# Performance work log

Hardware: AMD Instinct MI355X
Metric: run time of the kernel (lower is better)

## Reference

```python
import jax, jax.numpy as jnp
import numpy as np

N_NODES = 50000
N_EDGES = 800000
IN_DIM = 128
HID = 128
N_GRAPHS = 64


def setup_inputs() -> dict:
    key = jax.random.key(0)
    ks = jax.random.split(key, 12)
    edge_index = jax.random.randint(ks[0], (2, N_EDGES), 0, N_NODES, dtype=jnp.int64)
    edge_weight = jax.random.uniform(ks[1], (N_EDGES,), dtype=jnp.float32)
    input_feature = jax.random.normal(ks[2], (N_NODES, IN_DIM), dtype=jnp.float32)
    graph_indicator = jnp.sort(jax.random.randint(ks[3], (N_NODES,), 0, N_GRAPHS, dtype=jnp.int64))
    s = 0.05
    W1 = jax.random.normal(ks[4], (IN_DIM, HID), dtype=jnp.float32) * s
    b1 = jnp.zeros((HID,), jnp.float32)
    W2 = jax.random.normal(ks[5], (HID, HID), dtype=jnp.float32) * s
    b2 = jnp.zeros((HID,), jnp.float32)
    W3 = jax.random.normal(ks[6], (HID, HID), dtype=jnp.float32) * s
    b3 = jnp.zeros((HID,), jnp.float32)
    wa = jax.random.normal(ks[7], (3 * HID, 1), dtype=jnp.float32) * s
    ba = jnp.zeros((1,), jnp.float32)
    Wf = jax.random.normal(ks[8], (3 * HID * 2, IN_DIM), dtype=jnp.float32) * s
    bf = jnp.zeros((IN_DIM,), jnp.float32)
    return dict(edge_index=edge_index, edge_weight=edge_weight,
                input_feature=input_feature, graph_indicator=graph_indicator,
                W1=W1, b1=b1, W2=W2, b2=b2, W3=W3, b3=b3,
                wa=wa, ba=ba, Wf=Wf, bf=bf)


def reference(edge_index, edge_weight, input_feature, graph_indicator,
              W1, b1, W2, b2, W3, b3, wa, ba, Wf, bf):
    src, dst = edge_index[0], edge_index[1]

    def gcn(x, W, b):
        # GraphConvolution: adj @ (x @ W) + b, adj given as weighted edge list
        support = x @ W  # [N, d_out]
        msg = edge_weight[:, None] * support[src]  # [E, d_out] gather
        return jax.ops.segment_sum(msg, dst, num_segments=N_NODES) + b

    g1 = jax.nn.relu(gcn(input_feature, W1, b1))
    g2 = jax.nn.relu(gcn(g1, W2, b2))
    g3 = jax.nn.relu(gcn(g2, W3, b3))
    h = jnp.concatenate([g1, g2, g3], axis=1)  # [N, 3*HID]

    # SelfAttentionPooling: attention score via a 1-dim GraphConvolution, tanh gate
    score = jnp.tanh(gcn(h, wa, ba))  # [N, 1]
    pool = h * score

    # segment avg / max pooling per graph
    seg_sum = jax.ops.segment_sum(pool, graph_indicator, num_segments=N_GRAPHS)
    counts = jax.ops.segment_sum(jnp.ones((N_NODES, 1), pool.dtype), graph_indicator,
                                 num_segments=N_GRAPHS)
    avg = seg_sum / jnp.maximum(counts, 1.0)
    mx = jax.ops.segment_max(pool, graph_indicator, num_segments=N_GRAPHS)
    pooled = jnp.concatenate([avg, mx], axis=1)  # [G, 6*HID]

    return jax.nn.relu(pooled @ Wf + bf)  # [G, IN_DIM]
```

## Files before the change

kernel.cpp:

```cpp
#include <hip/hip_runtime.h>
#include <math.h>

#define HID 128
#define POOL_SEG 16
#define WT_STRIDE 136
#define ELL_D 48
#define SC_CHUNK 2048
#define FXS 16384.0f
#define FXI (1.0f/16384.0f)
#define FG_KC 12

typedef __attribute__((ext_vector_type(8))) short short8;
typedef __attribute__((ext_vector_type(4))) float float4v;

__device__ inline short f2bf(float f) {
  unsigned u = __builtin_bit_cast(unsigned, f);
  unsigned r = (u + 0x7fff + ((u >> 16) & 1)) >> 16;
  return (short)r;
}
__device__ inline unsigned pack2bf(float lo, float hi) {
  return (unsigned)(unsigned short)f2bf(lo) | ((unsigned)(unsigned short)f2bf(hi) << 16);
}
__device__ inline float bflo(unsigned u) { return __builtin_bit_cast(float, u << 16); }
__device__ inline float bfhi(unsigned u) { return __builtin_bit_cast(float, u & 0xffff0000u); }
__device__ inline float bf2f(unsigned short s) { return __builtin_bit_cast(float, (unsigned)s << 16); }

__global__ void detect_flags(const int* __restrict__ ei, const int* __restrict__ gi,
                             int* __restrict__ flags, int n_nodes) {
  if (blockIdx.x == 0 && threadIdx.x == 0) {
    int nz = 0;
    for (int i = 1; i < 64; i += 2) nz |= ei[i];
    flags[0] = (nz == 0) ? 1 : 0;
    flags[1] = (gi[n_nodes - 1] == 0) ? 1 : 0;
  }
}

__global__ void prep_edges(const void* __restrict__ ei_raw, const int* __restrict__ flags,
                           const float* __restrict__ ew, int* __restrict__ dst32,
                           int2* __restrict__ sw, int E) {
  int e = blockIdx.x * blockDim.x + threadIdx.x;
  if (e >= E) return;
  int s, d;
  if (flags[0]) {
    const long long* p = (const long long*)ei_raw;
    s = (int)p[e]; d = (int)p[E + e];
  } else {
    const int* p = (const int*)ei_raw;
    s = p[e]; d = p[E + e];
  }
  dst32[e] = d;
  sw[e] = make_int2(s, __builtin_bit_cast(int, ew[e]));
}

__global__ void scatter_ell(const int* __restrict__ dst32, const int2* __restrict__ sw,
                            int* __restrict__ cursor, int2* __restrict__ ell, int E, int N) {
  int group = blockIdx.x & 7;
  int chunk = blockIdx.x >> 3;
  int rng = (N + 7) / 8;
  int lo = group * rng;
  int hi = lo + rng; if (hi > N) hi = N;
  int base = chunk * SC_CHUNK;
  for (int i = 0; i < SC_CHUNK; i += 256) {
    int e = base + i + threadIdx.x;
    if (e < E) {
      int d = dst32[e];
      if (d >= lo && d < hi) {
        int2 r = sw[e];
        int pos = atomicAdd(&cursor[d], 1);
        if (pos < ELL_D)
          ell[(size_t)d * ELL_D + pos] = r;
      }
    }
  }
}

__global__ void convert_w(const float* __restrict__ W1, const float* __restrict__ W2,
                          const float* __restrict__ W3, short* __restrict__ T1,
                          short* __restrict__ T2, short* __restrict__ T3) {
  int i = blockIdx.x * blockDim.x + threadIdx.x;
  int which = i >> 14, idx = i & 16383;
  int k = idx >> 7, n = idx & 127;
  const float* W = (which == 0) ? W1 : ((which == 1) ? W2 : W3);
  short* T = (which == 0) ? T1 : ((which == 1) ? T2 : T3);
  T[n * WT_STRIDE + k] = f2bf(W[idx]);
}

__global__ __launch_bounds__(256) void gemm_mfma(const float* __restrict__ Af,
                                                 const unsigned short* __restrict__ Abf,
                                                 const short* __restrict__ Wt,
                                                 unsigned short* __restrict__ C,
                                                 int n, int a_is_bf16) {
  __shared__ short Wlds[128 * WT_STRIDE];
  int t = threadIdx.x;
  {
    const ulonglong2* gsrc = (const ulonglong2*)Wt;
    ulonglong2* ldst = (ulonglong2*)Wlds;
    for (int i = t; i < (128 * WT_STRIDE) / 8; i += 256) ldst[i] = gsrc[i];
  }
  __syncthreads();

  int wave = t >> 6, lane = t & 63;
  int quad = lane >> 4, l15 = lane & 15;
  int m0 = blockIdx.x * 64 + wave * 16;

  int m = m0 + l15; if (m >= n) m = n - 1;
  short8 afrag[4];
  if (a_is_bf16) {
    const unsigned short* Arow = Abf + (size_t)m * 128;
#pragma unroll
    for (int c = 0; c < 4; c++) afrag[c] = *(const short8*)(Arow + c * 32 + quad * 8);
  } else {
    const float* Arow = Af + (size_t)m * 128;
#pragma unroll
    for (int c = 0; c < 4; c++) {
      int k0 = c * 32 + quad * 8;
      float4 x = *(const float4*)(Arow + k0);
      float4 y = *(const float4*)(Arow + k0 + 4);
      short8 a;
      a[0] = f2bf(x.x); a[1] = f2bf(x.y); a[2] = f2bf(x.z); a[3] = f2bf(x.w);
      a[4] = f2bf(y.x); a[5] = f2bf(y.y); a[6] = f2bf(y.z); a[7] = f2bf(y.w);
      afrag[c] = a;
    }
  }

  float4v acc[8];
#pragma unroll
  for (int tt = 0; tt < 8; tt++) acc[tt] = (float4v){0.f, 0.f, 0.f, 0.f};

#pragma unroll
  for (int c = 0; c < 4; c++) {
    int kb = c * 32 + quad * 8;
#pragma unroll
    for (int tt = 0; tt < 8; tt++) {
      const short8* bp = (const short8*)&Wlds[(tt * 16 + l15) * WT_STRIDE + kb];
      acc[tt] = __builtin_amdgcn_mfma_f32_16x16x32_bf16(afrag[c], *bp, acc[tt], 0, 0, 0);
    }
  }

  int rbase = m0 + quad * 4;
#pragma unroll
  for (int tt = 0; tt < 8; tt++) {
    int col = tt * 16 + l15;
#pragma unroll
    for (int r = 0; r < 4; r++) {
      int row = rbase + r;
      if (row < n) C[(size_t)row * 128 + col] = (unsigned short)f2bf(acc[tt][r]);
    }
  }
}

__global__ void aggregate(const unsigned short* __restrict__ support,
                          const int* __restrict__ deg_arr,
                          const int2* __restrict__ ell,
                          const float* __restrict__ bias, unsigned short* __restrict__ out,
                          const unsigned short* __restrict__ g1p,
                          const unsigned short* __restrict__ g2p,
                          const float* __restrict__ wa,
                          float* __restrict__ s_pre,
                          int n, int do_score) {
  int gid = blockIdx.x * blockDim.x + threadIdx.x;
  int node = gid >> 4, q = gid & 15;
  if (node >= n) return;
  int deg = deg_arr[node]; if (deg > ELL_D) deg = ELL_D;
  const int2* row = ell + (size_t)node * ELL_D;
  int acc[8];
#pragma unroll
  for (int j = 0; j < 8; j++) acc[j] = 0;
  const uint4* s4 = (const uint4*)support;

  int i = 0;
  for (; i + 3 < deg; i += 4) {
    int2 r0 = row[i], r1 = row[i + 1], r2 = row[i + 2], r3 = row[i + 3];
    float w0 = __builtin_bit_cast(float, r0.y) * FXS;
    float w1 = __builtin_bit_cast(float, r1.y) * FXS;
    float w2 = __builtin_bit_cast(float, r2.y) * FXS;
    float w3 = __builtin_bit_cast(float, r3.y) * FXS;
    uint4 v0 = s4[(size_t)r0.x * 16 + q];
    uint4 v1 = s4[(size_t)r1.x * 16 + q];
    uint4 v2 = s4[(size_t)r2.x * 16 + q];
    uint4 v3 = s4[(size_t)r3.x * 16 + q];
    acc[0] += __float2int_rn(w0 * bflo(v0.x)); acc[1] += __float2int_rn(w0 * bfhi(v0.x));
    acc[2] += __float2int_rn(w0 * bflo(v0.y)); acc[3] += __float2int_rn(w0 * bfhi(v0.y));
    acc[4] += __float2int_rn(w0 * bflo(v0.z)); acc[5] += __float2int_rn(w0 * bfhi(v0.z));
    acc[6] += __float2int_rn(w0 * bflo(v0.w)); acc[7] += __float2int_rn(w0 * bfhi(v0.w));
    acc[0] += __float2int_rn(w1 * bflo(v1.x)); acc[1] += __float2int_rn(w1 * bfhi(v1.x));
    acc[2] += __float2int_rn(w1 * bflo(v1.y)); acc[3] += __float2int_rn(w1 * bfhi(v1.y));
    acc[4] += __float2int_rn(w1 * bflo(v1.z)); acc[5] += __float2int_rn(w1 * bfhi(v1.z));
    acc[6] += __float2int_rn(w1 * bflo(v1.w)); acc[7] += __float2int_rn(w1 * bfhi(v1.w));
    acc[0] += __float2int_rn(w2 * bflo(v2.x)); acc[1] += __float2int_rn(w2 * bfhi(v2.x));
    acc[2] += __float2int_rn(w2 * bflo(v2.y)); acc[3] += __float2int_rn(w2 * bfhi(v2.y));
    acc[4] += __float2int_rn(w2 * bflo(v2.z)); acc[5] += __float2int_rn(w2 * bfhi(v2.z));
    acc[6] += __float2int_rn(w2 * bflo(v2.w)); acc[7] += __float2int_rn(w2 * bfhi(v2.w));
    acc[0] += __float2int_rn(w3 * bflo(v3.x)); acc[1] += __float2int_rn(w3 * bfhi(v3.x));
    acc[2] += __float2int_rn(w3 * bflo(v3.y)); acc[3] += __float2int_rn(w3 * bfhi(v3.y));
    acc[4] += __float2int_rn(w3 * bflo(v3.z)); acc[5] += __float2int_rn(w3 * bfhi(v3.z));
    acc[6] += __float2int_rn(w3 * bflo(v3.w)); acc[7] += __float2int_rn(w3 * bfhi(v3.w));
  }
  for (; i < deg; i++) {
    int2 r0 = row[i];
    float w0 = __builtin_bit_cast(float, r0.y) * FXS;
    uint4 v0 = s4[(size_t)r0.x * 16 + q];
    acc[0] += __float2int_rn(w0 * bflo(v0.x)); acc[1] += __float2int_rn(w0 * bfhi(v0.x));
    acc[2] += __float2int_rn(w0 * bflo(v0.y)); acc[3] += __float2int_rn(w0 * bfhi(v0.y));
    acc[4] += __float2int_rn(w0 * bflo(v0.z)); acc[5] += __float2int_rn(w0 * bfhi(v0.z));
    acc[6] += __float2int_rn(w0 * bflo(v0.w)); acc[7] += __float2int_rn(w0 * bfhi(v0.w));
  }

  float f[8];
#pragma unroll
  for (int j = 0; j < 8; j++) f[j] = (float)acc[j] * FXI;

  float4 b0 = ((const float4*)bias)[q * 2];
  float4 b1 = ((const float4*)bias)[q * 2 + 1];
  f[0] = fmaxf(f[0] + b0.x, 0.f); f[1] = fmaxf(f[1] + b0.y, 0.f);
  f[2] = fmaxf(f[2] + b0.z, 0.f); f[3] = fmaxf(f[3] + b0.w, 0.f);
  f[4] = fmaxf(f[4] + b1.x, 0.f); f[5] = fmaxf(f[5] + b1.y, 0.f);
  f[6] = fmaxf(f[6] + b1.z, 0.f); f[7] = fmaxf(f[7] + b1.w, 0.f);

  uint4 o;
  o.x = pack2bf(f[0], f[1]); o.y = pack2bf(f[2], f[3]);
  o.z = pack2bf(f[4], f[5]); o.w = pack2bf(f[6], f[7]);
  ((uint4*)out)[(size_t)node * 16 + q] = o;

  if (do_score) {
    int d0 = q * 8;
    uint4 u1 = ((const uint4*)g1p)[(size_t)node * 16 + q];
    uint4 u2 = ((const uint4*)g2p)[(size_t)node * 16 + q];
    const float* wa1 = wa + d0;
    const float* wa2 = wa + 128 + d0;
    const float* wa3 = wa + 256 + d0;
    float sc = bflo(u1.x) * wa1[0] + bfhi(u1.x) * wa1[1]
             + bflo(u1.y) * wa1[2] + bfhi(u1.y) * wa1[3]
             + bflo(u1.z) * wa1[4] + bfhi(u1.z) * wa1[5]
             + bflo(u1.w) * wa1[6] + bfhi(u1.w) * wa1[7]
             + bflo(u2.x) * wa2[0] + bfhi(u2.x) * wa2[1]
             + bflo(u2.y) * wa2[2] + bfhi(u2.y) * wa2[3]
             + bflo(u2.z) * wa2[4] + bfhi(u2.z) * wa2[5]
             + bflo(u2.w) * wa2[6] + bfhi(u2.w) * wa2[7];
#pragma unroll
    for (int j = 0; j < 8; j++) sc += f[j] * wa3[j];
#pragma unroll
    for (int m = 1; m < 16; m <<= 1) sc += __shfl_xor(sc, m, 64);
    if (q == 0) s_pre[node] = sc;
  }
}

__global__ void att_aggregate(const float* __restrict__ s_pre, const int* __restrict__ deg_arr,
                              const int2* __restrict__ ell,
                              const float* __restrict__ ba, float* __restrict__ score, int n) {
  int node = blockIdx.x * blockDim.x + threadIdx.x;
  if (node >= n) return;
  int deg = deg_arr[node]; if (deg > ELL_D) deg = ELL_D;
  const int2* row = ell + (size_t)node * ELL_D;
  int acc = 0;
  for (int i = 0; i < deg; i++) {
    int2 r = row[i];
    acc += __float2int_rn(__builtin_bit_cast(float, r.y) * FXS * s_pre[r.x]);
  }
  score[node] = tanhf((float)acc * FXI + ba[0]);
}

__global__ void graph_bounds(const void* __restrict__ gi_raw, const int* __restrict__ flags,
                             int* __restrict__ gstart, int n, int ngraphs) {
  int g = threadIdx.x;
  if (g > ngraphs) return;
  if (g == ngraphs) { gstart[g] = n; return; }
  bool is64 = flags[1] != 0;
  const long long* g64 = (const long long*)gi_raw;
  const int* g32 = (const int*)gi_raw;
  int lo = 0, hi = n;
  while (lo < hi) {
    int mid = (lo + hi) >> 1;
    long long v = is64 ? g64[mid] : (long long)g32[mid];
    if (v < (long long)g) lo = mid + 1; else hi = mid;
  }
  gstart[g] = lo;
}

__global__ __launch_bounds__(384) void pool_partial(const unsigned short* __restrict__ g1,
                                                    const unsigned short* __restrict__ g2,
                                                    const unsigned short* __restrict__ g3,
                                                    const float* __restrict__ score,
                                                    const int* __restrict__ gstart,
                                                    float* __restrict__ part) {
  int g = blockIdx.x / POOL_SEG, seg = blockIdx.x % POOL_SEG;
  int d = threadIdx.x;
  int sg = d >> 7, dd = d & 127;
  const unsigned short* gp = (sg == 0) ? g1 : ((sg == 1) ? g2 : g3);
  int s = gstart[g], e = gstart[g + 1];
  int len = e - s;
  int chunk = (len + POOL_SEG - 1) / POOL_SEG;
  int ns = s + seg * chunk;
  int ne = ns + chunk; if (ne > e) ne = e;
  float sum = 0.f, mx = -3.402823466e38f;
  for (int node = ns; node < ne; node++) {
    float sc = score[node];
    float v = bf2f(gp[(size_t)node * 128 + dd]) * sc;
    sum += v;
    mx = fmaxf(mx, v);
  }
  size_t base = (size_t)blockIdx.x * 768;
  part[base + d] = sum;
  part[base + 384 + d] = mx;
}

__global__ __launch_bounds__(384) void pool_combine(const float* __restrict__ part,
                                                    const int* __restrict__ gstart,
                                                    float* __restrict__ pooled) {
  int g = blockIdx.x;
  int d = threadIdx.x;
  float sum = 0.f, mx = -3.402823466e38f;
  for (int seg = 0; seg < POOL_SEG; seg++) {
    size_t base = ((size_t)g * POOL_SEG + seg) * 768;
    sum += part[base + d];
    mx = fmaxf(mx, part[base + 384 + d]);
  }
  float cnt = (float)(gstart[g + 1] - gstart[g]);
  pooled[(size_t)g * 768 + d] = sum / fmaxf(cnt, 1.0f);
  pooled[(size_t)g * 768 + 384 + d] = mx;
}

__global__ __launch_bounds__(128) void fg_partial(const float* __restrict__ pooled,
                                                  const float* __restrict__ Wf,
                                                  float* __restrict__ fgp) {
  int g = blockIdx.x / FG_KC, kc = blockIdx.x % FG_KC;
  int c = threadIdx.x;
  __shared__ float row[64];
  if (c < 64) row[c] = pooled[(size_t)g * 768 + kc * 64 + c];
  __syncthreads();
  const float* Wp = Wf + (size_t)kc * 64 * 128 + c;
  float acc = 0.f;
#pragma unroll 8
  for (int k = 0; k < 64; k++) acc += row[k] * Wp[k * 128];
  fgp[((size_t)g * FG_KC + kc) * 128 + c] = acc;
}

__global__ __launch_bounds__(128) void fg_combine(const float* __restrict__ fgp,
                                                  const float* __restrict__ bf,
                                                  float* __restrict__ out) {
  int g = blockIdx.x;
  int c = threadIdx.x;
  float acc = bf[c];
#pragma unroll
  for (int kc = 0; kc < FG_KC; kc++)
    acc += fgp[((size_t)g * FG_KC + kc) * 128 + c];
  out[(size_t)g * 128 + c] = fmaxf(acc, 0.f);
}

extern "C" void kernel_launch(void* const* d_in, const int* in_sizes, int n_in,
                              void* d_out, int out_size, void* d_ws, size_t ws_size,
                              hipStream_t stream) {
  const void* ei_raw = d_in[0];
  const float* ew    = (const float*)d_in[1];
  const float* X     = (const float*)d_in[2];
  const void* gi_raw = d_in[3];
  const float* W1 = (const float*)d_in[4];  const float* b1 = (const float*)d_in[5];
  const float* W2 = (const float*)d_in[6];  const float* b2 = (const float*)d_in[7];
  const float* W3 = (const float*)d_in[8];  const float* b3 = (const float*)d_in[9];
  const float* wa = (const float*)d_in[10]; const float* ba = (const float*)d_in[11];
  const float* Wf = (const float*)d_in[12]; const float* bf = (const float*)d_in[13];
  float* out = (float*)d_out;

  const int E = in_sizes[1];
  const int N = in_sizes[2] / 128;
  const int G = out_size / 128;

  char* ws = (char*)d_ws;
  size_t off = 0;
  auto take = [&](size_t bytes) {
    char* p = ws + off;
    off = (off + bytes + 255) & ~(size_t)255;
    return p;
  };
  int*   flags   = (int*)take(16);
  int*   cursor  = (int*)take((size_t)N * 4);
  int*   dst32   = (int*)take((size_t)E * 4);
  int2*  sw      = (int2*)take((size_t)E * 8);
  int2*  ell     = (int2*)take((size_t)N * ELL_D * 8);
  short* wt1     = (short*)take((size_t)128 * WT_STRIDE * 2);
  short* wt2     = (short*)take((size_t)128 * WT_STRIDE * 2);
  short* wt3     = (short*)take((size_t)128 * WT_STRIDE * 2);
  unsigned short* support = (unsigned short*)take((size_t)N * 128 * 2);
  unsigned short* g1      = (unsigned short*)take((size_t)N * 128 * 2);
  unsigned short* g2      = (unsigned short*)take((size_t)N * 128 * 2);
  unsigned short* g3      = (unsigned short*)take((size_t)N * 128 * 2);
  float* s_pre   = (float*)take((size_t)N * 4);
  float* score   = (float*)take((size_t)N * 4);
  int*   gstart  = (int*)take((size_t)(G + 1) * 4);
  float* part    = (float*)take((size_t)G * POOL_SEG * 768 * 4);
  float* pooled  = (float*)take((size_t)G * 768 * 4);
  float* fgp     = (float*)take((size_t)G * FG_KC * 128 * 4);
  if (off > ws_size) return;

  hipMemsetAsync(cursor, 0, (size_t)N * 4, stream);
  detect_flags<<<1, 64, 0, stream>>>((const int*)ei_raw, (const int*)gi_raw, flags, N);
  prep_edges<<<(E + 255) / 256, 256, 0, stream>>>(ei_raw, flags, ew, dst32, sw, E);
  convert_w<<<(3 * 16384 + 255) / 256, 256, 0, stream>>>(W1, W2, W3, wt1, wt2, wt3);
  {
    int chunks = (E + SC_CHUNK - 1) / SC_CHUNK;
    scatter_ell<<<8 * chunks, 256, 0, stream>>>(dst32, sw, cursor, ell, E, N);
  }

  const int GB = (N + 63) / 64;
  const int AB = (N * 16 + 255) / 256;
  gemm_mfma<<<GB, 256, 0, stream>>>(X, (const unsigned short*)nullptr, wt1, support, N, 0);
  aggregate<<<AB, 256, 0, stream>>>(support, cursor, ell, b1, g1,
                                    nullptr, nullptr, nullptr, nullptr, N, 0);
  gemm_mfma<<<GB, 256, 0, stream>>>((const float*)nullptr, g1, wt2, support, N, 1);
  aggregate<<<AB, 256, 0, stream>>>(support, cursor, ell, b2, g2,
                                    nullptr, nullptr, nullptr, nullptr, N, 0);
  gemm_mfma<<<GB, 256, 0, stream>>>((const float*)nullptr, g2, wt3, support, N, 1);
  aggregate<<<AB, 256, 0, stream>>>(support, cursor, ell, b3, g3,
                                    g1, g2, wa, s_pre, N, 1);

  att_aggregate<<<(N + 255) / 256, 256, 0, stream>>>(s_pre, cursor, ell, ba, score, N);

  graph_bounds<<<1, 128, 0, stream>>>(gi_raw, flags, gstart, N, G);
  pool_partial<<<G * POOL_SEG, 384, 0, stream>>>(g1, g2, g3, score, gstart, part);
  pool_combine<<<G, 384, 0, stream>>>(part, gstart, pooled);
  fg_partial<<<G * FG_KC, 128, 0, stream>>>(pooled, Wf, fgp);
  fg_combine<<<G, 128, 0, stream>>>(fgp, bf, out);
}
```

Baseline: 323.6 us.

## Bin edges by destination group before ELL scatter and double GEMM rows per wave

Replaces the edge prep kernel and the 8-way filtered scatter with a binning kernel. It packs group, source and local destination into one word and writes each edge into a per-group bucket, so each scatter block reads only edges that belong to its group instead of rescanning the whole edge list eight times. Separately, the GEMM now has each wave compute 32 rows using two A fragments against each LDS B fragment, halving the grid and reusing W loads. The packing assumes source indices fit in 16 bits and local destinations in 13 bits, which holds for 50000 nodes but not in general.

```diff
diff --git a/kernel.cpp b/kernel.cpp
--- a/kernel.cpp
+++ b/kernel.cpp
@@ -9,6 +9,9 @@
 #define FXS 16384.0f
 #define FXI (1.0f/16384.0f)
 #define FG_KC 12
+#define BIN_TPB 256
+#define BIN_EPT 16
+#define BIN_EPB (BIN_TPB * BIN_EPT)
 
 typedef __attribute__((ext_vector_type(8))) short short8;
 typedef __attribute__((ext_vector_type(4))) float float4v;
@@ -35,41 +38,68 @@
   }
 }
 
-__global__ void prep_edges(const void* __restrict__ ei_raw, const int* __restrict__ flags,
-                           const float* __restrict__ ew, int* __restrict__ dst32,
-                           int2* __restrict__ sw, int E) {
-  int e = blockIdx.x * blockDim.x + threadIdx.x;
-  if (e >= E) return;
-  int s, d;
-  if (flags[0]) {
-    const long long* p = (const long long*)ei_raw;
-    s = (int)p[e]; d = (int)p[E + e];
-  } else {
-    const int* p = (const int*)ei_raw;
-    s = p[e]; d = p[E + e];
-  }
-  dst32[e] = d;
-  sw[e] = make_int2(s, __builtin_bit_cast(int, ew[e]));
-}
-
-__global__ void scatter_ell(const int* __restrict__ dst32, const int2* __restrict__ sw,
-                            int* __restrict__ cursor, int2* __restrict__ ell, int E, int N) {
+__global__ __launch_bounds__(BIN_TPB) void bin_edges(const void* __restrict__ ei_raw,
+                                                     const int* __restrict__ flags,
+                                                     const float* __restrict__ ew,
+                                                     int* __restrict__ gcur,
+                                                     int2* __restrict__ binned, int E, int N) {
+  __shared__ int cnt[8], base_s[8], loc[8];
+  int t = threadIdx.x;
+  if (t < 8) { cnt[t] = 0; loc[t] = 0; }
+  __syncthreads();
+  int rng = (N + 7) >> 3;
+  bool is64 = flags[0] != 0;
+  const long long* p64 = (const long long*)ei_raw;
+  const int* p32 = (const int*)ei_raw;
+  unsigned pk[BIN_EPT];
+  float wv[BIN_EPT];
+  int base = blockIdx.x * BIN_EPB;
+#pragma unroll
+  for (int j = 0; j < BIN_EPT; j++) {
+    int e = base + j * BIN_TPB + t;
+    pk[j] = 0xFFFFFFFFu;
+    if (e < E) {
+      int s = is64 ? (int)p64[e] : p32[e];
+      int d = is64 ? (int)p64[E + e] : p32[E + e];
+      int g = d / rng;
+      pk[j] = ((unsigned)g << 29) | ((unsigned)s << 13) | (unsigned)(d - g * rng);
+      wv[j] = ew[e];
+      atomicAdd(&cnt[g], 1);
+    }
+  }
+  __syncthreads();
+  if (t < 8) base_s[t] = atomicAdd(&gcur[t], cnt[t]);
+  __syncthreads();
+#pragma unroll
+  for (int j = 0; j < BIN_EPT; j++) {
+    if (pk[j] != 0xFFFFFFFFu) {
+      int g = pk[j] >> 29;
+      int pos = atomicAdd(&loc[g], 1);
+      binned[(size_t)g * E + base_s[g] + pos] =
+          make_int2((int)pk[j], __builtin_bit_cast(int, wv[j]));
+    }
+  }
+}
+
+__global__ void scatter_ell2(const int2* __restrict__ binned, const int* __restrict__ gcnt,
+                             int* __restrict__ cursor, int2* __restrict__ ell, int E, int N) {
   int group = blockIdx.x & 7;
   int chunk = blockIdx.x >> 3;
-  int rng = (N + 7) / 8;
+  int cnt = gcnt[group];
+  int base = chunk * SC_CHUNK;
+  if (base >= cnt) return;
+  int rng = (N + 7) >> 3;
   int lo = group * rng;
-  int hi = lo + rng; if (hi > N) hi = N;
-  int base = chunk * SC_CHUNK;
+  const int2* src = binned + (size_t)group * E;
   for (int i = 0; i < SC_CHUNK; i += 256) {
-    int e = base + i + threadIdx.x;
-    if (e < E) {
-      int d = dst32[e];
-      if (d >= lo && d < hi) {
-        int2 r = sw[e];
-        int pos = atomicAdd(&cursor[d], 1);
-        if (pos < ELL_D)
-          ell[(size_t)d * ELL_D + pos] = r;
-      }
+    int idx = base + i + threadIdx.x;
+    if (idx < cnt) {
+      int2 rec = src[idx];
+      int d = lo + (rec.x & 8191);
+      int s = (rec.x >> 13) & 0xFFFF;
+      int pos = atomicAdd(&cursor[d], 1);
+      if (pos < ELL_D)
+        ell[(size_t)d * ELL_D + pos] = make_int2(s, rec.y);
     }
   }
 }
@@ -101,50 +131,59 @@
 
   int wave = t >> 6, lane = t & 63;
   int quad = lane >> 4, l15 = lane & 15;
-  int m0 = blockIdx.x * 64 + wave * 16;
-
-  int m = m0 + l15; if (m >= n) m = n - 1;
-  short8 afrag[4];
-  if (a_is_bf16) {
-    const unsigned short* Arow = Abf + (size_t)m * 128;
-#pragma unroll
-    for (int c = 0; c < 4; c++) afrag[c] = *(const short8*)(Arow + c * 32 + quad * 8);
-  } else {
-    const float* Arow = Af + (size_t)m * 128;
-#pragma unroll
-    for (int c = 0; c < 4; c++) {
-      int k0 = c * 32 + quad * 8;
-      float4 x = *(const float4*)(Arow + k0);
-      float4 y = *(const float4*)(Arow + k0 + 4);
-      short8 a;
-      a[0] = f2bf(x.x); a[1] = f2bf(x.y); a[2] = f2bf(x.z); a[3] = f2bf(x.w);
-      a[4] = f2bf(y.x); a[5] = f2bf(y.y); a[6] = f2bf(y.z); a[7] = f2bf(y.w);
-      afrag[c] = a;
-    }
-  }
-
-  float4v acc[8];
-#pragma unroll
-  for (int tt = 0; tt < 8; tt++) acc[tt] = (float4v){0.f, 0.f, 0.f, 0.f};
+  int m0 = blockIdx.x * 128 + wave * 32;
+
+  short8 afrag[2][4];
+#pragma unroll
+  for (int rs = 0; rs < 2; rs++) {
+    int m = m0 + rs * 16 + l15; if (m >= n) m = n - 1;
+    if (a_is_bf16) {
+      const unsigned short* Arow = Abf + (size_t)m * 128;
+#pragma unroll
+      for (int c = 0; c < 4; c++) afrag[rs][c] = *(const short8*)(Arow + c * 32 + quad * 8);
+    } else {
+      const float* Arow = Af + (size_t)m * 128;
+#pragma unroll
+      for (int c = 0; c < 4; c++) {
+        int k0 = c * 32 + quad * 8;
+        float4 x = *(const float4*)(Arow + k0);
+        float4 y = *(const float4*)(Arow + k0 + 4);
+        short8 a;
+        a[0] = f2bf(x.x); a[1] = f2bf(x.y); a[2] = f2bf(x.z); a[3] = f2bf(x.w);
+        a[4] = f2bf(y.x); a[5] = f2bf(y.y); a[6] = f2bf(y.z); a[7] = f2bf(y.w);
+        afrag[rs][c] = a;
+      }
+    }
+  }
+
+  float4v acc[2][8];
+#pragma unroll
+  for (int rs = 0; rs < 2; rs++)
+#pragma unroll
+    for (int tt = 0; tt < 8; tt++) acc[rs][tt] = (float4v){0.f, 0.f, 0.f, 0.f};
 
 #pragma unroll
   for (int c = 0; c < 4; c++) {
     int kb = c * 32 + quad * 8;
 #pragma unroll
     for (int tt = 0; tt < 8; tt++) {
-      const short8* bp = (const short8*)&Wlds[(tt * 16 + l15) * WT_STRIDE + kb];
-      acc[tt] = __builtin_amdgcn_mfma_f32_16x16x32_bf16(afrag[c], *bp, acc[tt], 0, 0, 0);
-    }
-  }
-
-  int rbase = m0 + quad * 4;
-#pragma unroll
-  for (int tt = 0; tt < 8; tt++) {
-    int col = tt * 16 + l15;
-#pragma unroll
-    for (int r = 0; r < 4; r++) {
-      int row = rbase + r;
-      if (row < n) C[(size_t)row * 128 + col] = (unsigned short)f2bf(acc[tt][r]);
+      short8 b = *(const short8*)&Wlds[(tt * 16 + l15) * WT_STRIDE + kb];
+      acc[0][tt] = __builtin_amdgcn_mfma_f32_16x16x32_bf16(afrag[0][c], b, acc[0][tt], 0, 0, 0);
+      acc[1][tt] = __builtin_amdgcn_mfma_f32_16x16x32_bf16(afrag[1][c], b, acc[1][tt], 0, 0, 0);
+    }
+  }
+
+#pragma unroll
+  for (int rs = 0; rs < 2; rs++) {
+    int rbase = m0 + rs * 16 + quad * 4;
+#pragma unroll
+    for (int tt = 0; tt < 8; tt++) {
+      int col = tt * 16 + l15;
+#pragma unroll
+      for (int r = 0; r < 4; r++) {
+        int row = rbase + r;
+        if (row < n) C[(size_t)row * 128 + col] = (unsigned short)f2bf(acc[rs][tt][r]);
+      }
     }
   }
 }
@@ -373,9 +412,9 @@
     return p;
   };
   int*   flags   = (int*)take(16);
-  int*   cursor  = (int*)take((size_t)N * 4);
-  int*   dst32   = (int*)take((size_t)E * 4);
-  int2*  sw      = (int2*)take((size_t)E * 8);
+  int*   cursor  = (int*)take((size_t)(N + 8) * 4);
+  int*   gcur    = cursor + N;
+  int2*  binned  = (int2*)take((size_t)8 * E * 8);
   int2*  ell     = (int2*)take((size_t)N * ELL_D * 8);
   short* wt1     = (short*)take((size_t)128 * WT_STRIDE * 2);
   short* wt2     = (short*)take((size_t)128 * WT_STRIDE * 2);
@@ -392,16 +431,17 @@
   float* fgp     = (float*)take((size_t)G * FG_KC * 128 * 4);
   if (off > ws_size) return;
 
-  hipMemsetAsync(cursor, 0, (size_t)N * 4, stream);
+  hipMemsetAsync(cursor, 0, (size_t)(N + 8) * 4, stream);
   detect_flags<<<1, 64, 0, stream>>>((const int*)ei_raw, (const int*)gi_raw, flags, N);
-  prep_edges<<<(E + 255) / 256, 256, 0, stream>>>(ei_raw, flags, ew, dst32, sw, E);
   convert_w<<<(3 * 16384 + 255) / 256, 256, 0, stream>>>(W1, W2, W3, wt1, wt2, wt3);
+  bin_edges<<<(E + BIN_EPB - 1) / BIN_EPB, BIN_TPB, 0, stream>>>(ei_raw, flags, ew,
+                                                                 gcur, binned, E, N);
   {
     int chunks = (E + SC_CHUNK - 1) / SC_CHUNK;
-    scatter_ell<<<8 * chunks, 256, 0, stream>>>(dst32, sw, cursor, ell, E, N);
-  }
-
-  const int GB = (N + 63) / 64;
+    scatter_ell2<<<8 * chunks, 256, 0, stream>>>(binned, gcur, cursor, ell, E, N);
+  }
+
+  const int GB = (N + 127) / 128;
   const int AB = (N * 16 + 255) / 256;
   gemm_mfma<<<GB, 256, 0, stream>>>(X, (const unsigned short*)nullptr, wt1, support, N, 0);
   aggregate<<<AB, 256, 0, stream>>>(support, cursor, ell, b1, g1,
```

Result: slower. 333.2 us (+3.0%).
